# Kernel optimization log

Hardware: AMD Instinct MI355X
Metric: run time of the kernel (lower is better)

## Reference

```python
import jax, jax.numpy as jnp
import numpy as np

N_NODES = 50000
N_EDGES = 500000
IN_CH = 128
OUT_CH = 5
DIMS = [(IN_CH, 256), (256, 128), (128, 64)]
EPS = 1e-12  # F.normalize eps


def _lin_init(key, fan_out, fan_in):
    return jax.random.normal(key, (fan_out, fan_in), dtype=jnp.float32) * (1.0 / np.sqrt(fan_in))


def setup_inputs() -> dict:
    key = jax.random.key(0)
    ks = jax.random.split(key, 16)
    inp = {
        "x": jax.random.normal(ks[0], (N_NODES, IN_CH), dtype=jnp.float32),
        "edge_index": jax.random.randint(ks[1], (2, N_EDGES), 0, N_NODES, dtype=jnp.int64),
    }
    # SAGEConv params: lin_l (aggregated neighbors, with bias), lin_r (root, no bias)
    for i, (fi, fo) in enumerate(DIMS, start=1):
        inp[f"W{i}l"] = _lin_init(ks[3 * i], fo, fi)
        inp[f"b{i}"] = jnp.zeros((fo,), dtype=jnp.float32)
        inp[f"W{i}r"] = _lin_init(ks[3 * i + 1], fo, fi)
    inp["fcW"] = _lin_init(ks[13], OUT_CH, N_NODES * 64)
    inp["fcb"] = jnp.zeros((OUT_CH,), dtype=jnp.float32)
    return inp


def _sage(x, src, dst, Wl, bl, Wr):
    """PyG SAGEConv, aggr='mean', normalize=True: L2norm(lin_l(mean_j x_j) + lin_r(x_i))."""
    n = x.shape[0]
    agg = jax.ops.segment_sum(x[src], dst, num_segments=n)            # [N, F_in]
    deg = jax.ops.segment_sum(jnp.ones_like(src, dtype=x.dtype), dst, num_segments=n)
    mean = agg / jnp.clip(deg, 1.0)[:, None]
    out = mean @ Wl.T + bl + x @ Wr.T                                  # [N, F_out]
    nrm = jnp.linalg.norm(out, axis=-1, keepdims=True)
    return out / jnp.maximum(nrm, EPS)


def reference(x, edge_index, W1l, b1, W1r, W2l, b2, W2r, W3l, b3, W3r, fcW, fcb):
    src, dst = edge_index[0], edge_index[1]
    h = jax.nn.relu(_sage(x, src, dst, W1l, b1, W1r))
    h = jax.nn.relu(_sage(h, src, dst, W2l, b2, W2r))
    h = jax.nn.relu(_sage(h, src, dst, W3l, b3, W3r))
    logits = fcW @ h.reshape(-1) + fcb                                 # [OUT_CH]
    return jax.nn.softmax(logits, axis=-1)
```

## Files before the change

kernel.cpp:

```cpp
#include <hip/hip_runtime.h>
#include <hip/hip_bf16.h>
#include <math.h>

#define N_NODES 50000
#define N_EDGES 500000
#define FC_BLOCKS 1024

typedef __bf16 bf16x8 __attribute__((ext_vector_type(8)));
typedef float f32x4 __attribute__((ext_vector_type(4)));
typedef unsigned int u32x4 __attribute__((ext_vector_type(4)));

static __device__ __forceinline__ float bf2f_lo(unsigned int v) {
  return __uint_as_float(v << 16);
}
static __device__ __forceinline__ float bf2f_hi(unsigned int v) {
  return __uint_as_float(v & 0xffff0000u);
}
static __device__ __forceinline__ unsigned short f2bf(float f) {
  unsigned int u = __float_as_uint(f);
  return (unsigned short)((u + 0x7fffu + ((u >> 16) & 1u)) >> 16);
}
static __device__ __forceinline__ bf16x8 ld8(const unsigned short* p) {
  u32x4 u = *(const u32x4*)p;
  return __builtin_bit_cast(bf16x8, u);
}

__global__ void prep_kernel(const float* __restrict__ x, unsigned short* __restrict__ xb,
                            const float* __restrict__ W1l, const float* __restrict__ W1r,
                            unsigned short* __restrict__ w1b,
                            const float* __restrict__ W2l, const float* __restrict__ W2r,
                            unsigned short* __restrict__ w2b,
                            const float* __restrict__ W3l, const float* __restrict__ W3r,
                            unsigned short* __restrict__ w3b,
                            int* __restrict__ cntfill) {
  int idx = blockIdx.x * 256 + threadIdx.x;
  if (idx < 1600000) {
    float4 v = ((const float4*)x)[idx];
    ushort4 o;
    o.x = f2bf(v.x); o.y = f2bf(v.y); o.z = f2bf(v.z); o.w = f2bf(v.w);
    ((ushort4*)xb)[idx] = o;
  } else if (idx < 1665536) {
    int i = idx - 1600000;
    int j = i >> 8, k = i & 255;
    float v = (k < 128) ? W1l[j * 128 + k] : W1r[j * 128 + (k - 128)];
    w1b[i] = f2bf(v);
  } else if (idx < 1731072) {
    int i = idx - 1665536;
    int j = i >> 8, k = i & 255;
    float v = (j < 128) ? W2l[j * 256 + k] : W2r[(j - 128) * 256 + k];
    w2b[i] = f2bf(v);
  } else if (idx < 1747456) {
    int i = idx - 1731072;
    int j = i >> 7, k = i & 127;
    float v = (j < 64) ? W3l[j * 128 + k] : W3r[(j - 64) * 128 + k];
    w3b[i] = f2bf(v);
  } else if (idx < 1772456) {
    int i = idx - 1747456;
    ((int4*)cntfill)[i] = make_int4(0, 0, 0, 0);
  }
}

__global__ void hist_kernel(const int* __restrict__ dst, int* __restrict__ cnt) {
  int e = blockIdx.x * blockDim.x + threadIdx.x;
  if (e < N_EDGES) atomicAdd(&cnt[dst[e]], 1);
}

__global__ void chunk_sum_kernel(const int* __restrict__ cnt, int* __restrict__ bsum) {
  __shared__ int s[512];
  int i = blockIdx.x * 512 + threadIdx.x;
  s[threadIdx.x] = (i < N_NODES) ? cnt[i] : 0;
  __syncthreads();
  for (int off = 256; off > 0; off >>= 1) {
    if (threadIdx.x < off) s[threadIdx.x] += s[threadIdx.x + off];
    __syncthreads();
  }
  if (threadIdx.x == 0) bsum[blockIdx.x] = s[0];
}

__global__ void scan_final_kernel(const int* __restrict__ cnt, const int* __restrict__ bsum,
                                  int* __restrict__ row_ptr, float* __restrict__ inv_deg) {
  __shared__ int s[512];
  __shared__ int base_sh;
  int b = blockIdx.x;
  int t = threadIdx.x;
  if (t < 64) {
    int acc = 0;
    for (int i = t; i < b; i += 64) acc += bsum[i];
    #pragma unroll
    for (int m = 1; m <= 32; m <<= 1) acc += __shfl_xor(acc, m);
    if (t == 0) base_sh = acc;
  }
  int i = b * 512 + t;
  int v = (i < N_NODES) ? cnt[i] : 0;
  s[t] = v;
  __syncthreads();
  for (int off = 1; off < 512; off <<= 1) {
    int u = (t >= off) ? s[t - off] : 0;
    __syncthreads();
    s[t] += u;
    __syncthreads();
  }
  if (i < N_NODES) {
    row_ptr[i + 1] = base_sh + s[t];
    if (i == 0) row_ptr[0] = 0;
    inv_deg[i] = 1.0f / fmaxf((float)v, 1.0f);
  }
}

__global__ void fill_csr_kernel(const int* __restrict__ src, const int* __restrict__ dst,
                                const int* __restrict__ row_ptr, int* __restrict__ fill,
                                int* __restrict__ col) {
  int e = blockIdx.x * blockDim.x + threadIdx.x;
  if (e < N_EDGES) {
    int d = dst[e];
    int pos = row_ptr[d] + atomicAdd(&fill[d], 1);
    col[pos] = src[e];
  }
}

#define ACC8(v)                                          \
  do {                                                   \
    a[0] += bf2f_lo((v)[0]); a[1] += bf2f_hi((v)[0]);    \
    a[2] += bf2f_lo((v)[1]); a[3] += bf2f_hi((v)[1]);    \
    a[4] += bf2f_lo((v)[2]); a[5] += bf2f_hi((v)[2]);    \
    a[6] += bf2f_lo((v)[3]); a[7] += bf2f_hi((v)[3]);    \
  } while (0)

__global__ void agg_mean_bf16(const unsigned short* __restrict__ xb, const int* __restrict__ rp,
                              const int* __restrict__ cl, const float* __restrict__ idg,
                              unsigned short* __restrict__ out) {
  int node = blockIdx.x * 4 + (threadIdx.x >> 6);
  int lane = threadIdx.x & 63;
  int g = lane >> 4, l = lane & 15;
  int beg = rp[node], end = rp[node + 1];
  float a[8] = {0.f, 0.f, 0.f, 0.f, 0.f, 0.f, 0.f, 0.f};
  for (int e0 = beg; e0 < end; e0 += 8) {
    int e1 = e0 + g, e2 = e0 + 4 + g;
    if (e1 < end) {
      u32x4 v = *(const u32x4*)(xb + (size_t)cl[e1] * 128 + l * 8);
      ACC8(v);
    }
    if (e2 < end) {
      u32x4 v = *(const u32x4*)(xb + (size_t)cl[e2] * 128 + l * 8);
      ACC8(v);
    }
  }
  #pragma unroll
  for (int i = 0; i < 8; i++) {
    a[i] += __shfl_xor(a[i], 16);
    a[i] += __shfl_xor(a[i], 32);
  }
  if (g == 0) {
    float s = idg[node];
    u32x4 o;
    #pragma unroll
    for (int i = 0; i < 4; i++)
      o[i] = (unsigned int)f2bf(a[2 * i] * s) | ((unsigned int)f2bf(a[2 * i + 1] * s) << 16);
    *(u32x4*)(out + (size_t)node * 128 + l * 8) = o;
  }
}

__global__ void agg_nr128(const unsigned short* __restrict__ yl, const unsigned short* __restrict__ yr,
                          const float* __restrict__ bias, const int* __restrict__ rp,
                          const int* __restrict__ cl, const float* __restrict__ idg,
                          unsigned short* __restrict__ outb) {
  int node = blockIdx.x * 4 + (threadIdx.x >> 6);
  int lane = threadIdx.x & 63;
  int g = lane >> 4, l = lane & 15;
  int beg = rp[node], end = rp[node + 1];
  float a[8] = {0.f, 0.f, 0.f, 0.f, 0.f, 0.f, 0.f, 0.f};
  for (int e0 = beg; e0 < end; e0 += 8) {
    int e1 = e0 + g, e2 = e0 + 4 + g;
    if (e1 < end) {
      u32x4 v = *(const u32x4*)(yl + (size_t)cl[e1] * 128 + l * 8);
      ACC8(v);
    }
    if (e2 < end) {
      u32x4 v = *(const u32x4*)(yl + (size_t)cl[e2] * 128 + l * 8);
      ACC8(v);
    }
  }
  #pragma unroll
  for (int i = 0; i < 8; i++) {
    a[i] += __shfl_xor(a[i], 16);
    a[i] += __shfl_xor(a[i], 32);
  }
  float s = idg[node];
  u32x4 r = *(const u32x4*)(yr + (size_t)node * 128 + l * 8);
  float v[8];
  v[0] = a[0] * s + bias[l * 8 + 0] + bf2f_lo(r[0]);
  v[1] = a[1] * s + bias[l * 8 + 1] + bf2f_hi(r[0]);
  v[2] = a[2] * s + bias[l * 8 + 2] + bf2f_lo(r[1]);
  v[3] = a[3] * s + bias[l * 8 + 3] + bf2f_hi(r[1]);
  v[4] = a[4] * s + bias[l * 8 + 4] + bf2f_lo(r[2]);
  v[5] = a[5] * s + bias[l * 8 + 5] + bf2f_hi(r[2]);
  v[6] = a[6] * s + bias[l * 8 + 6] + bf2f_lo(r[3]);
  v[7] = a[7] * s + bias[l * 8 + 7] + bf2f_hi(r[3]);
  float p = 0.f;
  #pragma unroll
  for (int i = 0; i < 8; i++) p += v[i] * v[i];
  #pragma unroll
  for (int msk = 1; msk <= 8; msk <<= 1) p += __shfl_xor(p, msk);
  float sc = 1.0f / fmaxf(sqrtf(p), 1e-12f);
  if (g == 0) {
    u32x4 o;
    #pragma unroll
    for (int i = 0; i < 4; i++) {
      float w0 = fmaxf(v[2 * i] * sc, 0.f);
      float w1 = fmaxf(v[2 * i + 1] * sc, 0.f);
      o[i] = (unsigned int)f2bf(w0) | ((unsigned int)f2bf(w1) << 16);
    }
    *(u32x4*)(outb + (size_t)node * 128 + l * 8) = o;
  }
}

__global__ void agg_nr64(const unsigned short* __restrict__ yl, const unsigned short* __restrict__ yr,
                         const float* __restrict__ bias, const int* __restrict__ rp,
                         const int* __restrict__ cl, const float* __restrict__ idg,
                         float* __restrict__ outf) {
  int node = blockIdx.x * 4 + (threadIdx.x >> 6);
  int lane = threadIdx.x & 63;
  int g = lane >> 3, l = lane & 7;
  int beg = rp[node], end = rp[node + 1];
  float a[8] = {0.f, 0.f, 0.f, 0.f, 0.f, 0.f, 0.f, 0.f};
  for (int e0 = beg; e0 < end; e0 += 16) {
    int e1 = e0 + g, e2 = e0 + 8 + g;
    if (e1 < end) {
      u32x4 v = *(const u32x4*)(yl + (size_t)cl[e1] * 64 + l * 8);
      ACC8(v);
    }
    if (e2 < end) {
      u32x4 v = *(const u32x4*)(yl + (size_t)cl[e2] * 64 + l * 8);
      ACC8(v);
    }
  }
  #pragma unroll
  for (int i = 0; i < 8; i++) {
    a[i] += __shfl_xor(a[i], 8);
    a[i] += __shfl_xor(a[i], 16);
    a[i] += __shfl_xor(a[i], 32);
  }
  float s = idg[node];
  u32x4 r = *(const u32x4*)(yr + (size_t)node * 64 + l * 8);
  float v[8];
  v[0] = a[0] * s + bias[l * 8 + 0] + bf2f_lo(r[0]);
  v[1] = a[1] * s + bias[l * 8 + 1] + bf2f_hi(r[0]);
  v[2] = a[2] * s + bias[l * 8 + 2] + bf2f_lo(r[1]);
  v[3] = a[3] * s + bias[l * 8 + 3] + bf2f_hi(r[1]);
  v[4] = a[4] * s + bias[l * 8 + 4] + bf2f_lo(r[2]);
  v[5] = a[5] * s + bias[l * 8 + 5] + bf2f_hi(r[2]);
  v[6] = a[6] * s + bias[l * 8 + 6] + bf2f_lo(r[3]);
  v[7] = a[7] * s + bias[l * 8 + 7] + bf2f_hi(r[3]);
  float p = 0.f;
  #pragma unroll
  for (int i = 0; i < 8; i++) p += v[i] * v[i];
  #pragma unroll
  for (int msk = 1; msk <= 4; msk <<= 1) p += __shfl_xor(p, msk);
  float sc = 1.0f / fmaxf(sqrtf(p), 1e-12f);
  if (g == 0) {
    f32x4 o0, o1;
    #pragma unroll
    for (int i = 0; i < 4; i++) o0[i] = fmaxf(v[i] * sc, 0.f);
    #pragma unroll
    for (int i = 0; i < 4; i++) o1[i] = fmaxf(v[4 + i] * sc, 0.f);
    *(f32x4*)(outf + (size_t)node * 64 + l * 8) = o0;
    *(f32x4*)(outf + (size_t)node * 64 + l * 8 + 4) = o1;
  }
}

__launch_bounds__(512)
__global__ void gemm12_kernel(const unsigned short* __restrict__ A1,
                              const unsigned short* __restrict__ A2,
                              const unsigned short* __restrict__ W1, const float* __restrict__ b1,
                              const unsigned short* __restrict__ W2,
                              unsigned short* __restrict__ y2l, unsigned short* __restrict__ y2r) {
  __shared__ unsigned char As[64 * 512];
  __shared__ float sums[64][9];
  const int tid = threadIdx.x;
  const int wave = tid >> 6, lane = tid & 63;
  const int l15 = lane & 15, kg = lane >> 4;
  const int row0 = blockIdx.x * 64;
  const int wj = wave * 32;

  #pragma unroll
  for (int i = 0; i < 4; i++) {
    int boff = i * 8192 + tid * 16;
    int row = boff >> 9;
    int colb = boff & 511;
    int grow = row0 + row; if (grow >= N_NODES) grow = N_NODES - 1;
    u32x4 v;
    if (colb < 256) v = *(const u32x4*)((const char*)A1 + (size_t)grow * 256 + colb);
    else            v = *(const u32x4*)((const char*)A2 + (size_t)grow * 256 + colb - 256);
    *(u32x4*)(&As[row * 512 + (colb ^ ((row & 7) << 4))]) = v;
  }

  f32x4 acc[2][4];
  #pragma unroll
  for (int jf = 0; jf < 2; jf++)
    #pragma unroll
    for (int mf = 0; mf < 4; mf++) acc[jf][mf] = (f32x4){0.f, 0.f, 0.f, 0.f};

  const unsigned short* Wp1 = W1 + (size_t)(wj + l15) * 256 + kg * 8;
  bf16x8 wc[2], wn[2];
  #pragma unroll
  for (int jf = 0; jf < 2; jf++) wc[jf] = ld8(Wp1 + jf * 4096);

  __syncthreads();

  #pragma unroll
  for (int k0 = 0; k0 < 256; k0 += 32) {
    if (k0 < 224) {
      #pragma unroll
      for (int jf = 0; jf < 2; jf++) wn[jf] = ld8(Wp1 + jf * 4096 + k0 + 32);
    }
    bf16x8 af[4];
    int colb = (k0 + kg * 8) * 2;
    #pragma unroll
    for (int mf = 0; mf < 4; mf++) {
      int row = mf * 16 + l15;
      af[mf] = ld8((const unsigned short*)&As[row * 512 + (colb ^ ((row & 7) << 4))]);
    }
    #pragma unroll
    for (int jf = 0; jf < 2; jf++)
      #pragma unroll
      for (int mf = 0; mf < 4; mf++)
        acc[jf][mf] = __builtin_amdgcn_mfma_f32_16x16x32_bf16(wc[jf], af[mf], acc[jf][mf], 0, 0, 0);
    if (k0 < 224) {
      #pragma unroll
      for (int jf = 0; jf < 2; jf++) wc[jf] = wn[jf];
    }
  }

  {
    float p[4] = {0.f, 0.f, 0.f, 0.f};
    #pragma unroll
    for (int jf = 0; jf < 2; jf++)
      #pragma unroll
      for (int r = 0; r < 4; r++) {
        float bj = b1[wj + jf * 16 + kg * 4 + r];
        #pragma unroll
        for (int mf = 0; mf < 4; mf++) {
          float v = acc[jf][mf][r] + bj;
          acc[jf][mf][r] = v;
          p[mf] += v * v;
        }
      }
    #pragma unroll
    for (int mf = 0; mf < 4; mf++) {
      p[mf] += __shfl_xor(p[mf], 16);
      p[mf] += __shfl_xor(p[mf], 32);
    }
    if (kg == 0) {
      #pragma unroll
      for (int mf = 0; mf < 4; mf++) sums[mf * 16 + l15][wave] = p[mf];
    }
    __syncthreads();
    #pragma unroll
    for (int mf = 0; mf < 4; mf++) {
      int rl = mf * 16 + l15;
      float tot = 0.f;
      #pragma unroll
      for (int w = 0; w < 8; w++) tot += sums[rl][w];
      float sc = 1.0f / fmaxf(sqrtf(tot), 1e-12f);
      #pragma unroll
      for (int jf = 0; jf < 2; jf++)
        #pragma unroll
        for (int r = 0; r < 4; r++) acc[jf][mf][r] = fmaxf(acc[jf][mf][r] * sc, 0.f);
    }
  }

  __syncthreads();

  #pragma unroll
  for (int mf = 0; mf < 4; mf++) {
    int row = mf * 16 + l15;
    #pragma unroll
    for (int jf = 0; jf < 2; jf++) {
      ushort4 o;
      o.x = f2bf(acc[jf][mf][0]);
      o.y = f2bf(acc[jf][mf][1]);
      o.z = f2bf(acc[jf][mf][2]);
      o.w = f2bf(acc[jf][mf][3]);
      int colb = (wj + jf * 16 + kg * 4) * 2;
      *(ushort4*)(&As[row * 512 + (colb ^ ((row & 7) << 4))]) = o;
    }
  }
  const unsigned short* Wp2 = W2 + (size_t)(wj + l15) * 256 + kg * 8;
  #pragma unroll
  for (int jf = 0; jf < 2; jf++) wc[jf] = ld8(Wp2 + jf * 4096);
  #pragma unroll
  for (int jf = 0; jf < 2; jf++)
    #pragma unroll
    for (int mf = 0; mf < 4; mf++) acc[jf][mf] = (f32x4){0.f, 0.f, 0.f, 0.f};

  __syncthreads();

  #pragma unroll
  for (int k0 = 0; k0 < 256; k0 += 32) {
    if (k0 < 224) {
      #pragma unroll
      for (int jf = 0; jf < 2; jf++) wn[jf] = ld8(Wp2 + jf * 4096 + k0 + 32);
    }
    bf16x8 af[4];
    int colb = (k0 + kg * 8) * 2;
    #pragma unroll
    for (int mf = 0; mf < 4; mf++) {
      int row = mf * 16 + l15;
      af[mf] = ld8((const unsigned short*)&As[row * 512 + (colb ^ ((row & 7) << 4))]);
    }
    #pragma unroll
    for (int jf = 0; jf < 2; jf++)
      #pragma unroll
      for (int mf = 0; mf < 4; mf++)
        acc[jf][mf] = __builtin_amdgcn_mfma_f32_16x16x32_bf16(wc[jf], af[mf], acc[jf][mf], 0, 0, 0);
    if (k0 < 224) {
      #pragma unroll
      for (int jf = 0; jf < 2; jf++) wc[jf] = wn[jf];
    }
  }

  unsigned short* ob = (wj >= 128) ? y2r : y2l;
  int cb = wj & 127;
  #pragma unroll
  for (int mf = 0; mf < 4; mf++) {
    int m = row0 + mf * 16 + l15;
    if (m < N_NODES) {
      #pragma unroll
      for (int jf = 0; jf < 2; jf++) {
        ushort4 o;
        o.x = f2bf(acc[jf][mf][0]);
        o.y = f2bf(acc[jf][mf][1]);
        o.z = f2bf(acc[jf][mf][2]);
        o.w = f2bf(acc[jf][mf][3]);
        *(ushort4*)&ob[(size_t)m * 128 + cb + jf * 16 + kg * 4] = o;
      }
    }
  }
}

template<int FI, int FO, bool OSPLIT>
__launch_bounds__(512)
__global__ void mfma_gemm(const unsigned short* __restrict__ A1,
                          const unsigned short* __restrict__ W,
                          unsigned short* __restrict__ outA, unsigned short* __restrict__ outB) {
  constexpr int ROWB = FI * 2;
  constexpr int JF = FO / 128;
  __shared__ unsigned char As[64 * ROWB];
  const int tid = threadIdx.x;
  const int wave = tid >> 6, lane = tid & 63;
  const int l15 = lane & 15, kg = lane >> 4;
  const int row0 = blockIdx.x * 64;
  const int wj = wave * (FO / 8);

  #pragma unroll
  for (int i = 0; i < (64 * ROWB) / 8192; i++) {
    int boff = i * 8192 + tid * 16;
    int row = boff / ROWB;
    int colb = boff % ROWB;
    int grow = row0 + row; if (grow >= N_NODES) grow = N_NODES - 1;
    u32x4 v = *(const u32x4*)((const char*)A1 + (size_t)grow * ROWB + colb);
    *(u32x4*)(&As[row * ROWB + (colb ^ ((row & 7) << 4))]) = v;
  }

  f32x4 acc[JF][4];
  #pragma unroll
  for (int jf = 0; jf < JF; jf++)
    #pragma unroll
    for (int mf = 0; mf < 4; mf++) acc[jf][mf] = (f32x4){0.f, 0.f, 0.f, 0.f};

  const unsigned short* Wp = W + (size_t)(wj + l15) * FI + kg * 8;
  bf16x8 wc[JF], wn[JF];
  #pragma unroll
  for (int jf = 0; jf < JF; jf++) wc[jf] = ld8(Wp + (size_t)jf * 16 * FI);

  __syncthreads();

  #pragma unroll
  for (int k0 = 0; k0 < FI; k0 += 32) {
    if (k0 + 32 < FI) {
      #pragma unroll
      for (int jf = 0; jf < JF; jf++) wn[jf] = ld8(Wp + (size_t)jf * 16 * FI + k0 + 32);
    }
    bf16x8 af[4];
    int colb = (k0 + kg * 8) * 2;
    #pragma unroll
    for (int mf = 0; mf < 4; mf++) {
      int row = mf * 16 + l15;
      af[mf] = ld8((const unsigned short*)&As[row * ROWB + (colb ^ ((row & 7) << 4))]);
    }
    #pragma unroll
    for (int jf = 0; jf < JF; jf++)
      #pragma unroll
      for (int mf = 0; mf < 4; mf++)
        acc[jf][mf] = __builtin_amdgcn_mfma_f32_16x16x32_bf16(wc[jf], af[mf], acc[jf][mf], 0, 0, 0);
    if (k0 + 32 < FI) {
      #pragma unroll
      for (int jf = 0; jf < JF; jf++) wc[jf] = wn[jf];
    }
  }

  unsigned short* ob = outA;
  int cb = wj;
  constexpr int OSTR = OSPLIT ? FO / 2 : FO;
  if (OSPLIT && wj >= FO / 2) { ob = outB; cb = wj - FO / 2; }
  #pragma unroll
  for (int mf = 0; mf < 4; mf++) {
    int m = row0 + mf * 16 + l15;
    if (m < N_NODES) {
      #pragma unroll
      for (int jf = 0; jf < JF; jf++) {
        ushort4 o;
        o.x = f2bf(acc[jf][mf][0]);
        o.y = f2bf(acc[jf][mf][1]);
        o.z = f2bf(acc[jf][mf][2]);
        o.w = f2bf(acc[jf][mf][3]);
        *(ushort4*)&ob[(size_t)m * OSTR + cb + jf * 16 + kg * 4] = o;
      }
    }
  }
}

__global__ void fc_partial_kernel(const float* __restrict__ fcW, const float* __restrict__ h3,
                                  float* __restrict__ partial) {
  const size_t L = (size_t)N_NODES * 64;
  float acc[5] = {0.f, 0.f, 0.f, 0.f, 0.f};
  for (size_t i = (size_t)blockIdx.x * 256 + threadIdx.x; i < L; i += (size_t)gridDim.x * 256) {
    float h = h3[i];
    #pragma unroll
    for (int c = 0; c < 5; c++) acc[c] += h * fcW[(size_t)c * L + i];
  }
  __shared__ float red[4][5];
  #pragma unroll
  for (int msk = 1; msk <= 32; msk <<= 1)
    #pragma unroll
    for (int c = 0; c < 5; c++) acc[c] += __shfl_xor(acc[c], msk);
  int lane = threadIdx.x & 63, wave = threadIdx.x >> 6;
  if (lane == 0)
    #pragma unroll
    for (int c = 0; c < 5; c++) red[wave][c] = acc[c];
  __syncthreads();
  if (threadIdx.x < 5) {
    float s = red[0][threadIdx.x] + red[1][threadIdx.x] + red[2][threadIdx.x] + red[3][threadIdx.x];
    partial[blockIdx.x * 5 + threadIdx.x] = s;
  }
}

__global__ void fc_final_kernel(const float* __restrict__ partial, const float* __restrict__ fcb,
                                float* __restrict__ out) {
  __shared__ float red[4];
  __shared__ float logits[5];
  int tid = threadIdx.x;
  for (int c = 0; c < 5; c++) {
    float a = 0.f;
    for (int b = tid; b < FC_BLOCKS; b += 256) a += partial[b * 5 + c];
    #pragma unroll
    for (int msk = 1; msk <= 32; msk <<= 1) a += __shfl_xor(a, msk);
    if ((tid & 63) == 0) red[tid >> 6] = a;
    __syncthreads();
    if (tid == 0) logits[c] = red[0] + red[1] + red[2] + red[3] + fcb[c];
    __syncthreads();
  }
  if (tid == 0) {
    float mx = logits[0];
    for (int c = 1; c < 5; c++) mx = fmaxf(mx, logits[c]);
    float e[5], s = 0.f;
    for (int c = 0; c < 5; c++) { e[c] = expf(logits[c] - mx); s += e[c]; }
    for (int c = 0; c < 5; c++) out[c] = e[c] / s;
  }
}

extern "C" void kernel_launch(void* const* d_in, const int* in_sizes, int n_in,
                              void* d_out, int out_size, void* d_ws, size_t ws_size,
                              hipStream_t stream) {
  (void)in_sizes; (void)n_in; (void)out_size; (void)ws_size;
  const float* x   = (const float*)d_in[0];
  const int*   ei  = (const int*)d_in[1];
  const float* W1l = (const float*)d_in[2];
  const float* b1  = (const float*)d_in[3];
  const float* W1r = (const float*)d_in[4];
  const float* W2l = (const float*)d_in[5];
  const float* b2  = (const float*)d_in[6];
  const float* W2r = (const float*)d_in[7];
  const float* W3l = (const float*)d_in[8];
  const float* b3  = (const float*)d_in[9];
  const float* W3r = (const float*)d_in[10];
  const float* fcW = (const float*)d_in[11];
  const float* fcb = (const float*)d_in[12];
  const int* src = ei;
  const int* dst = ei + N_EDGES;

  char* ws = (char*)d_ws;
  size_t off = 0;
  auto alloc = [&](size_t bytes) { void* p = ws + off; off += (bytes + 255) & ~(size_t)255; return p; };
  int*   cntfill = (int*)alloc((size_t)100000 * 4);
  int*   row_ptr = (int*)alloc((size_t)(N_NODES + 1) * 4);
  int*   bsum    = (int*)alloc(512);
  float* inv_deg = (float*)alloc((size_t)N_NODES * 4);
  int*   col     = (int*)alloc((size_t)N_EDGES * 4);
  unsigned short* w1b = (unsigned short*)alloc((size_t)256 * 256 * 2);
  unsigned short* w2b = (unsigned short*)alloc((size_t)256 * 256 * 2);
  unsigned short* w3b = (unsigned short*)alloc((size_t)128 * 128 * 2);
  float* partial = (float*)alloc((size_t)FC_BLOCKS * 5 * 4);
  unsigned short* B0 = (unsigned short*)alloc((size_t)N_NODES * 128 * 2);
  unsigned short* B1 = (unsigned short*)alloc((size_t)N_NODES * 128 * 2);
  unsigned short* B2 = (unsigned short*)alloc((size_t)N_NODES * 256 * 2);
  unsigned short* B3 = (unsigned short*)alloc((size_t)N_NODES * 128 * 2);
  float* B4 = (float*)alloc((size_t)N_NODES * 64 * 4);
  float* out5 = (float*)d_out;

  int*   cnt  = cntfill;
  int*   fill = cntfill + N_NODES;
  unsigned short* xb    = B0;
  unsigned short* mean1 = B1;
  unsigned short* y2l   = B1;
  unsigned short* y2r   = B0;
  unsigned short* h2    = B3;
  unsigned short* y3l   = B2;
  unsigned short* y3r   = B2 + (size_t)N_NODES * 64;
  float*          h3f   = B4;

  const int NCH = (N_NODES + 511) / 512;

  prep_kernel<<<(1772456 + 255) / 256, 256, 0, stream>>>(
      x, xb, W1l, W1r, w1b, W2l, W2r, w2b, W3l, W3r, w3b, cntfill);

  hist_kernel<<<(N_EDGES + 255) / 256, 256, 0, stream>>>(dst, cnt);
  chunk_sum_kernel<<<NCH, 512, 0, stream>>>(cnt, bsum);
  scan_final_kernel<<<NCH, 512, 0, stream>>>(cnt, bsum, row_ptr, inv_deg);
  fill_csr_kernel<<<(N_EDGES + 255) / 256, 256, 0, stream>>>(src, dst, row_ptr, fill, col);

  const int AGB = N_NODES / 4;
  const int GB  = (N_NODES + 63) / 64;

  agg_mean_bf16<<<AGB, 256, 0, stream>>>(xb, row_ptr, col, inv_deg, mean1);
  gemm12_kernel<<<GB, 512, 0, stream>>>(mean1, xb, w1b, b1, w2b, y2l, y2r);
  agg_nr128<<<AGB, 256, 0, stream>>>(y2l, y2r, b2, row_ptr, col, inv_deg, h2);

  mfma_gemm<128, 128, true><<<GB, 512, 0, stream>>>(h2, w3b, y3l, y3r);
  agg_nr64<<<AGB, 256, 0, stream>>>(y3l, y3r, b3, row_ptr, col, inv_deg, h3f);

  fc_partial_kernel<<<FC_BLOCKS, 256, 0, stream>>>(fcW, h3f, partial);
  fc_final_kernel<<<1, 256, 0, stream>>>(partial, fcb, out5);
}
```

Before: 216.9 us.

## Use 128-row tiles with 2x4 wave grid in fused GEMM kernels

The fused layer-1/layer-2 GEMM and the layer-3 GEMM now process 128 rows per block, with waves arranged as two row groups by four column groups. This halves per-row weight fetches from global memory and doubles the A-tile reuse per wave. Global loads for the A tile are issued into registers before any LDS stores, and launch bounds request occupancy 4. The cost is twice the LDS per block (64KB in gemm12) and more accumulator registers, which may limit occupancy, and there are half as many blocks.

```diff
diff --git a/kernel.cpp b/kernel.cpp
--- a/kernel.cpp
+++ b/kernel.cpp
@@ -268,42 +268,50 @@
   }
 }
 
-__launch_bounds__(512)
+__launch_bounds__(512, 4)
 __global__ void gemm12_kernel(const unsigned short* __restrict__ A1,
                               const unsigned short* __restrict__ A2,
                               const unsigned short* __restrict__ W1, const float* __restrict__ b1,
                               const unsigned short* __restrict__ W2,
                               unsigned short* __restrict__ y2l, unsigned short* __restrict__ y2r) {
-  __shared__ unsigned char As[64 * 512];
-  __shared__ float sums[64][9];
+  __shared__ unsigned char As[128 * 512];
+  __shared__ float sums[128][9];
   const int tid = threadIdx.x;
   const int wave = tid >> 6, lane = tid & 63;
   const int l15 = lane & 15, kg = lane >> 4;
-  const int row0 = blockIdx.x * 64;
-  const int wj = wave * 32;
-
-  #pragma unroll
-  for (int i = 0; i < 4; i++) {
+  const int rg = wave >> 2, cg = wave & 3;
+  const int row0 = blockIdx.x * 128;
+  const int rbase = rg * 64;
+  const int cbase = cg * 64;
+
+  u32x4 sv[8];
+  #pragma unroll
+  for (int i = 0; i < 8; i++) {
     int boff = i * 8192 + tid * 16;
     int row = boff >> 9;
     int colb = boff & 511;
     int grow = row0 + row; if (grow >= N_NODES) grow = N_NODES - 1;
-    u32x4 v;
-    if (colb < 256) v = *(const u32x4*)((const char*)A1 + (size_t)grow * 256 + colb);
-    else            v = *(const u32x4*)((const char*)A2 + (size_t)grow * 256 + colb - 256);
-    *(u32x4*)(&As[row * 512 + (colb ^ ((row & 7) << 4))]) = v;
-  }
-
-  f32x4 acc[2][4];
-  #pragma unroll
-  for (int jf = 0; jf < 2; jf++)
+    if (colb < 256) sv[i] = *(const u32x4*)((const char*)A1 + (size_t)grow * 256 + colb);
+    else            sv[i] = *(const u32x4*)((const char*)A2 + (size_t)grow * 256 + colb - 256);
+  }
+  #pragma unroll
+  for (int i = 0; i < 8; i++) {
+    int boff = i * 8192 + tid * 16;
+    int row = boff >> 9;
+    int colb = boff & 511;
+    *(u32x4*)(&As[row * 512 + (colb ^ ((row & 7) << 4))]) = sv[i];
+  }
+
+  f32x4 acc[4][4];
+  #pragma unroll
+  for (int jf = 0; jf < 4; jf++)
     #pragma unroll
     for (int mf = 0; mf < 4; mf++) acc[jf][mf] = (f32x4){0.f, 0.f, 0.f, 0.f};
 
-  const unsigned short* Wp1 = W1 + (size_t)(wj + l15) * 256 + kg * 8;
-  bf16x8 wc[2], wn[2];
-  #pragma unroll
-  for (int jf = 0; jf < 2; jf++) wc[jf] = ld8(Wp1 + jf * 4096);
+  const unsigned short* Wp1 = W1 + (size_t)(cbase + l15) * 256 + kg * 8;
+  bf16x8 wc[4], wn[4];
+  #pragma unroll
+  for (int jf = 0; jf < 4; jf++) wc[jf] = ld8(Wp1 + jf * 4096);
 
   __syncthreads();
 
@@ -311,33 +319,33 @@
   for (int k0 = 0; k0 < 256; k0 += 32) {
     if (k0 < 224) {
       #pragma unroll
-      for (int jf = 0; jf < 2; jf++) wn[jf] = ld8(Wp1 + jf * 4096 + k0 + 32);
-    }
+      for (int jf = 0; jf < 4; jf++) wn[jf] = ld8(Wp1 + jf * 4096 + k0 + 32);
+    }
+    int colb = (k0 + kg * 8) * 2;
     bf16x8 af[4];
-    int colb = (k0 + kg * 8) * 2;
     #pragma unroll
     for (int mf = 0; mf < 4; mf++) {
-      int row = mf * 16 + l15;
+      int row = rbase + mf * 16 + l15;
       af[mf] = ld8((const unsigned short*)&As[row * 512 + (colb ^ ((row & 7) << 4))]);
     }
     #pragma unroll
-    for (int jf = 0; jf < 2; jf++)
+    for (int jf = 0; jf < 4; jf++)
       #pragma unroll
       for (int mf = 0; mf < 4; mf++)
         acc[jf][mf] = __builtin_amdgcn_mfma_f32_16x16x32_bf16(wc[jf], af[mf], acc[jf][mf], 0, 0, 0);
     if (k0 < 224) {
       #pragma unroll
-      for (int jf = 0; jf < 2; jf++) wc[jf] = wn[jf];
+      for (int jf = 0; jf < 4; jf++) wc[jf] = wn[jf];
     }
   }
 
   {
     float p[4] = {0.f, 0.f, 0.f, 0.f};
     #pragma unroll
-    for (int jf = 0; jf < 2; jf++)
+    for (int jf = 0; jf < 4; jf++)
       #pragma unroll
       for (int r = 0; r < 4; r++) {
-        float bj = b1[wj + jf * 16 + kg * 4 + r];
+        float bj = b1[cbase + jf * 16 + kg * 4 + r];
         #pragma unroll
         for (int mf = 0; mf < 4; mf++) {
           float v = acc[jf][mf][r] + bj;
@@ -352,18 +360,17 @@
     }
     if (kg == 0) {
       #pragma unroll
-      for (int mf = 0; mf < 4; mf++) sums[mf * 16 + l15][wave] = p[mf];
+      for (int mf = 0; mf < 4; mf++) sums[rbase + mf * 16 + l15][wave] = p[mf];
     }
     __syncthreads();
     #pragma unroll
     for (int mf = 0; mf < 4; mf++) {
-      int rl = mf * 16 + l15;
-      float tot = 0.f;
-      #pragma unroll
-      for (int w = 0; w < 8; w++) tot += sums[rl][w];
+      int rl = rbase + mf * 16 + l15;
+      float tot = sums[rl][rg * 4 + 0] + sums[rl][rg * 4 + 1] +
+                  sums[rl][rg * 4 + 2] + sums[rl][rg * 4 + 3];
       float sc = 1.0f / fmaxf(sqrtf(tot), 1e-12f);
       #pragma unroll
-      for (int jf = 0; jf < 2; jf++)
+      for (int jf = 0; jf < 4; jf++)
         #pragma unroll
         for (int r = 0; r < 4; r++) acc[jf][mf][r] = fmaxf(acc[jf][mf][r] * sc, 0.f);
     }
@@ -373,23 +380,23 @@
 
   #pragma unroll
   for (int mf = 0; mf < 4; mf++) {
-    int row = mf * 16 + l15;
-    #pragma unroll
-    for (int jf = 0; jf < 2; jf++) {
+    int row = rbase + mf * 16 + l15;
+    #pragma unroll
+    for (int jf = 0; jf < 4; jf++) {
       ushort4 o;
       o.x = f2bf(acc[jf][mf][0]);
       o.y = f2bf(acc[jf][mf][1]);
       o.z = f2bf(acc[jf][mf][2]);
       o.w = f2bf(acc[jf][mf][3]);
-      int colb = (wj + jf * 16 + kg * 4) * 2;
+      int colb = (cbase + jf * 16 + kg * 4) * 2;
       *(ushort4*)(&As[row * 512 + (colb ^ ((row & 7) << 4))]) = o;
     }
   }
-  const unsigned short* Wp2 = W2 + (size_t)(wj + l15) * 256 + kg * 8;
-  #pragma unroll
-  for (int jf = 0; jf < 2; jf++) wc[jf] = ld8(Wp2 + jf * 4096);
-  #pragma unroll
-  for (int jf = 0; jf < 2; jf++)
+  const unsigned short* Wp2 = W2 + (size_t)(cbase + l15) * 256 + kg * 8;
+  #pragma unroll
+  for (int jf = 0; jf < 4; jf++) wc[jf] = ld8(Wp2 + jf * 4096);
+  #pragma unroll
+  for (int jf = 0; jf < 4; jf++)
     #pragma unroll
     for (int mf = 0; mf < 4; mf++) acc[jf][mf] = (f32x4){0.f, 0.f, 0.f, 0.f};
 
@@ -399,34 +406,34 @@
   for (int k0 = 0; k0 < 256; k0 += 32) {
     if (k0 < 224) {
       #pragma unroll
-      for (int jf = 0; jf < 2; jf++) wn[jf] = ld8(Wp2 + jf * 4096 + k0 + 32);
-    }
+      for (int jf = 0; jf < 4; jf++) wn[jf] = ld8(Wp2 + jf * 4096 + k0 + 32);
+    }
+    int colb = (k0 + kg * 8) * 2;
     bf16x8 af[4];
-    int colb = (k0 + kg * 8) * 2;
     #pragma unroll
     for (int mf = 0; mf < 4; mf++) {
-      int row = mf * 16 + l15;
+      int row = rbase + mf * 16 + l15;
       af[mf] = ld8((const unsigned short*)&As[row * 512 + (colb ^ ((row & 7) << 4))]);
     }
     #pragma unroll
-    for (int jf = 0; jf < 2; jf++)
+    for (int jf = 0; jf < 4; jf++)
       #pragma unroll
       for (int mf = 0; mf < 4; mf++)
         acc[jf][mf] = __builtin_amdgcn_mfma_f32_16x16x32_bf16(wc[jf], af[mf], acc[jf][mf], 0, 0, 0);
     if (k0 < 224) {
       #pragma unroll
-      for (int jf = 0; jf < 2; jf++) wc[jf] = wn[jf];
-    }
-  }
-
-  unsigned short* ob = (wj >= 128) ? y2r : y2l;
-  int cb = wj & 127;
+      for (int jf = 0; jf < 4; jf++) wc[jf] = wn[jf];
+    }
+  }
+
+  unsigned short* ob = (cg >= 2) ? y2r : y2l;
+  int cb = (cg & 1) * 64;
   #pragma unroll
   for (int mf = 0; mf < 4; mf++) {
-    int m = row0 + mf * 16 + l15;
+    int m = row0 + rbase + mf * 16 + l15;
     if (m < N_NODES) {
       #pragma unroll
-      for (int jf = 0; jf < 2; jf++) {
+      for (int jf = 0; jf < 4; jf++) {
         ushort4 o;
         o.x = f2bf(acc[jf][mf][0]);
         o.y = f2bf(acc[jf][mf][1]);
@@ -439,39 +446,47 @@
 }
 
 template<int FI, int FO, bool OSPLIT>
-__launch_bounds__(512)
+__launch_bounds__(512, 4)
 __global__ void mfma_gemm(const unsigned short* __restrict__ A1,
                           const unsigned short* __restrict__ W,
                           unsigned short* __restrict__ outA, unsigned short* __restrict__ outB) {
   constexpr int ROWB = FI * 2;
-  constexpr int JF = FO / 128;
-  __shared__ unsigned char As[64 * ROWB];
+  __shared__ unsigned char As[128 * ROWB];
   const int tid = threadIdx.x;
   const int wave = tid >> 6, lane = tid & 63;
   const int l15 = lane & 15, kg = lane >> 4;
-  const int row0 = blockIdx.x * 64;
-  const int wj = wave * (FO / 8);
-
-  #pragma unroll
-  for (int i = 0; i < (64 * ROWB) / 8192; i++) {
+  const int rg = wave >> 2, cg = wave & 3;
+  const int row0 = blockIdx.x * 128;
+  const int rbase = rg * 64;
+  const int cbase = cg * (FO / 4);
+
+  u32x4 sv[4];
+  #pragma unroll
+  for (int i = 0; i < 4; i++) {
     int boff = i * 8192 + tid * 16;
     int row = boff / ROWB;
     int colb = boff % ROWB;
     int grow = row0 + row; if (grow >= N_NODES) grow = N_NODES - 1;
-    u32x4 v = *(const u32x4*)((const char*)A1 + (size_t)grow * ROWB + colb);
-    *(u32x4*)(&As[row * ROWB + (colb ^ ((row & 7) << 4))]) = v;
-  }
-
-  f32x4 acc[JF][4];
-  #pragma unroll
-  for (int jf = 0; jf < JF; jf++)
+    sv[i] = *(const u32x4*)((const char*)A1 + (size_t)grow * ROWB + colb);
+  }
+  #pragma unroll
+  for (int i = 0; i < 4; i++) {
+    int boff = i * 8192 + tid * 16;
+    int row = boff / ROWB;
+    int colb = boff % ROWB;
+    *(u32x4*)(&As[row * ROWB + (colb ^ ((row & 7) << 4))]) = sv[i];
+  }
+
+  f32x4 acc[2][4];
+  #pragma unroll
+  for (int jf = 0; jf < 2; jf++)
     #pragma unroll
     for (int mf = 0; mf < 4; mf++) acc[jf][mf] = (f32x4){0.f, 0.f, 0.f, 0.f};
 
-  const unsigned short* Wp = W + (size_t)(wj + l15) * FI + kg * 8;
-  bf16x8 wc[JF], wn[JF];
-  #pragma unroll
-  for (int jf = 0; jf < JF; jf++) wc[jf] = ld8(Wp + (size_t)jf * 16 * FI);
+  const unsigned short* Wp = W + (size_t)(cbase + l15) * FI + kg * 8;
+  bf16x8 wc[2], wn[2];
+  #pragma unroll
+  for (int jf = 0; jf < 2; jf++) wc[jf] = ld8(Wp + (size_t)jf * 16 * FI);
 
   __syncthreads();
 
@@ -479,36 +494,36 @@
   for (int k0 = 0; k0 < FI; k0 += 32) {
     if (k0 + 32 < FI) {
       #pragma unroll
-      for (int jf = 0; jf < JF; jf++) wn[jf] = ld8(Wp + (size_t)jf * 16 * FI + k0 + 32);
-    }
+      for (int jf = 0; jf < 2; jf++) wn[jf] = ld8(Wp + (size_t)jf * 16 * FI + k0 + 32);
+    }
+    int colb = (k0 + kg * 8) * 2;
     bf16x8 af[4];
-    int colb = (k0 + kg * 8) * 2;
     #pragma unroll
     for (int mf = 0; mf < 4; mf++) {
-      int row = mf * 16 + l15;
+      int row = rbase + mf * 16 + l15;
       af[mf] = ld8((const unsigned short*)&As[row * ROWB + (colb ^ ((row & 7) << 4))]);
     }
     #pragma unroll
-    for (int jf = 0; jf < JF; jf++)
+    for (int jf = 0; jf < 2; jf++)
       #pragma unroll
       for (int mf = 0; mf < 4; mf++)
         acc[jf][mf] = __builtin_amdgcn_mfma_f32_16x16x32_bf16(wc[jf], af[mf], acc[jf][mf], 0, 0, 0);
     if (k0 + 32 < FI) {
       #pragma unroll
-      for (int jf = 0; jf < JF; jf++) wc[jf] = wn[jf];
+      for (int jf = 0; jf < 2; jf++) wc[jf] = wn[jf];
     }
   }
 
   unsigned short* ob = outA;
-  int cb = wj;
+  int cb = cbase;
   constexpr int OSTR = OSPLIT ? FO / 2 : FO;
-  if (OSPLIT && wj >= FO / 2) { ob = outB; cb = wj - FO / 2; }
+  if (OSPLIT && cbase >= FO / 2) { ob = outB; cb = cbase - FO / 2; }
   #pragma unroll
   for (int mf = 0; mf < 4; mf++) {
-    int m = row0 + mf * 16 + l15;
+    int m = row0 + rbase + mf * 16 + l15;
     if (m < N_NODES) {
       #pragma unroll
-      for (int jf = 0; jf < JF; jf++) {
+      for (int jf = 0; jf < 2; jf++) {
         ushort4 o;
         o.x = f2bf(acc[jf][mf][0]);
         o.y = f2bf(acc[jf][mf][1]);
@@ -630,13 +645,13 @@
   fill_csr_kernel<<<(N_EDGES + 255) / 256, 256, 0, stream>>>(src, dst, row_ptr, fill, col);
 
   const int AGB = N_NODES / 4;
-  const int GB  = (N_NODES + 63) / 64;
+  const int GB12 = (N_NODES + 127) / 128;
 
   agg_mean_bf16<<<AGB, 256, 0, stream>>>(xb, row_ptr, col, inv_deg, mean1);
-  gemm12_kernel<<<GB, 512, 0, stream>>>(mean1, xb, w1b, b1, w2b, y2l, y2r);
+  gemm12_kernel<<<GB12, 512, 0, stream>>>(mean1, xb, w1b, b1, w2b, y2l, y2r);
   agg_nr128<<<AGB, 256, 0, stream>>>(y2l, y2r, b2, row_ptr, col, inv_deg, h2);
 
-  mfma_gemm<128, 128, true><<<GB, 512, 0, stream>>>(h2, w3b, y3l, y3r);
+  mfma_gemm<128, 128, true><<<GB12, 512, 0, stream>>>(h2, w3b, y3l, y3r);
   agg_nr64<<<AGB, 256, 0, stream>>>(y3l, y3r, b3, row_ptr, col, inv_deg, h3f);
 
   fc_partial_kernel<<<FC_BLOCKS, 256, 0, stream>>>(fcW, h3f, partial);
```

New measurement: 218.7 us. Within noise of the previous version (+0.8%).
